# Kernel optimization log

Hardware: AMD Instinct MI355X
Metric: run time of the kernel (lower is better)

## Reference

```python
import jax, jax.numpy as jnp
import numpy as np

NEG = -9e9  # large negative used by the original torch code for masking


def setup_inputs() -> dict:
    key = jax.random.key(0)
    k1, k2, k3, k4 = jax.random.split(key, 4)
    B, N, L, D = 64, 128, 64, 768
    return {
        "text_embeddings": jax.random.normal(k1, (B, N, D), dtype=jnp.float32),
        "image_embeddings": jax.random.normal(k2, (B, L, D), dtype=jnp.float32),
        "text_mask": jax.random.randint(k3, (B, N), 0, 2, dtype=jnp.int32),
        "image_mask": jax.random.randint(k4, (B, L), 0, 2, dtype=jnp.int32),
    }


def _grounding(text_emb, image_emb, text_mask, image_mask):
    # Vectorized version of the B x B python loop in score_grounding.
    tm = text_mask.astype(text_emb.dtype)   # [B, N]
    im = image_mask.astype(text_emb.dtype)  # [B, L]
    # pairwise mask: mask[i, j, n, l] = text_mask[i, n] * image_mask[j, l]
    mask = tm[:, None, :, None] * im[None, :, None, :]            # [B, B, N, L]
    att = jnp.einsum('ind,jld->ijnl', text_emb, image_emb) * mask  # [B, B, N, L]
    att = jnp.where(att * mask != 0, att, NEG)
    # softmax over image spans (last dim), masked
    aw_first = jax.nn.softmax(att, axis=-1) * mask
    score1 = (aw_first * att).sum(-1).mean(-1)                     # [B, B]
    # softmax over text spans (dim 2 == the N axis), masked (transpose trick in torch)
    aw_second = jax.nn.softmax(att, axis=2) * mask
    score2 = (aw_second * att).sum(-1).mean(-1)                    # [B, B]
    sent_scores = score1 + score2                                  # [B, B]
    B = text_emb.shape[0]
    idx = jnp.arange(B)
    token_scores = att[idx, idx]                                   # diagonal pairs, [B, N, L]
    return sent_scores, token_scores


def reference(text_embeddings, image_embeddings, text_mask, image_mask):
    B = text_embeddings.shape[0]
    S, token_scores = _grounding(text_embeddings, image_embeddings, text_mask, image_mask)
    # text_emb_i2s = softmax(att_weights) @ image_emb
    text_emb_i2s = jnp.einsum('bnl,bld->bnd', jax.nn.softmax(token_scores, axis=-1), image_embeddings)
    # loss = -(sum diag logsoftmax(S, dim=1) + sum diag logsoftmax(S.T, dim=1)) / n
    ls1 = jnp.diagonal(jax.nn.log_softmax(S, axis=1))
    ls2 = jnp.diagonal(jax.nn.log_softmax(S.T, axis=1))
    loss = -(jnp.sum(ls1) + jnp.sum(ls2)) / B
    return loss, text_emb_i2s
```

## Files before the change

### kernel.cpp

```cpp
#include <hip/hip_runtime.h>
#include <math.h>

#define BSZ 64
#define NN  128
#define LL  64
#define DD  768
#define NEGV (-9e9f)

#define TQ (BSZ * NN * DD / 4)
#define IQ (BSZ * LL * DD / 4)

typedef _Float16 f16x8 __attribute__((ext_vector_type(8)));
typedef __attribute__((ext_vector_type(4))) float f32x4;

__device__ __forceinline__ void gl_lds16(const void* g, void* l) {
    __builtin_amdgcn_global_load_lds(
        (const __attribute__((address_space(1))) void*)g,
        (__attribute__((address_space(3))) void*)l, 16, 0, 0);
}

__global__ __launch_bounds__(256) void k_prep(
    const float4* __restrict__ t4, const float4* __restrict__ g4,
    ushort4* __restrict__ A, ushort4* __restrict__ B)
{
    int id = blockIdx.x * 256 + threadIdx.x;
    const float4* src; ushort4* dst; int idx;
    if (id < TQ) { src = t4; dst = A; idx = id; }
    else         { src = g4; dst = B; idx = id - TQ; }
    float4 x = src[idx];
    _Float16 h0 = (_Float16)x.x, h1 = (_Float16)x.y;
    _Float16 h2 = (_Float16)x.z, h3 = (_Float16)x.w;
    ushort4 o;
    o.x = __builtin_bit_cast(unsigned short, h0);
    o.y = __builtin_bit_cast(unsigned short, h1);
    o.z = __builtin_bit_cast(unsigned short, h2);
    o.w = __builtin_bit_cast(unsigned short, h3);
    dst[idx] = o;
}

__device__ __forceinline__ void stage_chunk(
    const unsigned short* __restrict__ pa, const unsigned short* __restrict__ pb,
    int k0, char* buf, int wave, int lane)
{
    int rsub = lane >> 3;
    int k8s  = lane & 7;
#pragma unroll
    for (int c = 0; c < 4; c++) {
        int r  = c * 32 + wave * 8 + rsub;
        int k8 = k8s ^ (r & 7);
        gl_lds16(pa + (size_t)r * DD + k0 + k8 * 8, buf + c * 4096 + wave * 1024);
        gl_lds16(pb + (size_t)r * DD + k0 + k8 * 8, buf + 16384 + c * 4096 + wave * 1024);
    }
}

__global__ __launch_bounds__(256, 2) void k_scores(
    const unsigned short* __restrict__ A, const unsigned short* __restrict__ B,
    const int* __restrict__ tmask, const int* __restrict__ imask,
    float* __restrict__ S, float* __restrict__ W)
{
    union SmemU {
        char  stage[2][32768];
        float Cs[NN][129];
    };
    __shared__ SmemU u;
    __shared__ float tmi[NN];
    __shared__ float imj[NN];
    __shared__ float rowred[256];
    __shared__ float colred[NN];
    __shared__ float rowm[256], rowsm[256];
    __shared__ float colm[256], colp1[256], colp2[256];

    const int bid = blockIdx.x;
    const int grp = bid >> 4, idx = bid & 15;
    const int i  = (grp >> 3) * 4 + (idx >> 2);
    const int jj = (grp & 7) * 4 + (idx & 3);
    const int j0 = jj * 2;

    const int tid  = threadIdx.x;
    const int wave = tid >> 6;
    const int lane = tid & 63;
    const int quad = lane >> 4;
    const int l15  = lane & 15;
    const int rh   = wave & 1;
    const int ch   = wave >> 1;

    if (tid < NN) {
        tmi[tid] = tmask[i * NN + tid] ? 1.f : 0.f;
        imj[tid] = imask[j0 * LL + tid] ? 1.f : 0.f;
    }

    const unsigned short* pa = A + (size_t)i * NN * DD;
    const unsigned short* pb = B + (size_t)j0 * LL * DD;

    f32x4 acc[4][4];
    const f32x4 zf = {0.f, 0.f, 0.f, 0.f};
#pragma unroll
    for (int tr = 0; tr < 4; tr++)
#pragma unroll
        for (int tc = 0; tc < 4; tc++) acc[tr][tc] = zf;

    stage_chunk(pa, pb, 0, u.stage[0], wave, lane);
    __syncthreads();

    for (int c = 0; c < 12; c++) {
        if (c + 1 < 12)
            stage_chunk(pa, pb, (c + 1) << 6, u.stage[(c + 1) & 1], wave, lane);
        const char* Ab = u.stage[c & 1];
        const char* Bb = Ab + 16384;
#pragma unroll
        for (int s = 0; s < 2; s++) {
            int k8q = s * 4 + quad;
            int sw  = k8q ^ (l15 & 7);
            f16x8 af[4], bfr[4];
#pragma unroll
            for (int t = 0; t < 4; t++) {
                int row = rh * 64 + t * 16 + l15;
                af[t]  = *(const f16x8*)(Ab + ((row << 3) + sw) * 16);
                int col = ch * 64 + t * 16 + l15;
                bfr[t] = *(const f16x8*)(Bb + ((col << 3) + sw) * 16);
            }
#pragma unroll
            for (int tr = 0; tr < 4; tr++)
#pragma unroll
                for (int tc = 0; tc < 4; tc++)
                    acc[tr][tc] = __builtin_amdgcn_mfma_f32_16x16x32_f16(
                        af[tr], bfr[tc], acc[tr][tc], 0, 0, 0);
        }
        __syncthreads();
    }

#pragma unroll
    for (int tr = 0; tr < 4; tr++) {
        int rb = rh * 64 + tr * 16 + quad * 4;
#pragma unroll
        for (int tc = 0; tc < 4; tc++) {
            int col = ch * 64 + tc * 16 + l15;
            float im = imj[col];
#pragma unroll
            for (int rr = 0; rr < 4; rr++) {
                int row = rb + rr;
                float v = acc[tr][tc][rr];
                bool keep = (tmi[row] != 0.f) && (im != 0.f) && (v != 0.f);
                u.Cs[row][col] = keep ? v : NEGV;
            }
        }
    }
    __syncthreads();

    {
        int jh = tid >> 7, n = tid & 127;
        const float* Crow = &u.Cs[n][jh * 64];
        float m = -INFINITY;
        for (int l = 0; l < LL; l++) m = fmaxf(m, Crow[l]);
        float ssum = 0.f, ws = 0.f;
        for (int l = 0; l < LL; l++) {
            float v = Crow[l];
            float e = __expf(v - m);
            ssum += e;
            ws += imj[jh * 64 + l] * e * v;
        }
        rowm[tid] = m;
        rowsm[tid] = ssum;
        rowred[tid] = tmi[n] * (ws / ssum);
    }
    __syncthreads();

    {
        int c  = tid & 127;
        int n0 = (tid >> 7) * 64;
        float m = -INFINITY;
        for (int n = n0; n < n0 + 64; n++) m = fmaxf(m, u.Cs[n][c]);
        colm[tid] = m;
        __syncthreads();
        m = fmaxf(colm[tid], colm[tid ^ 128]);
        float ssum = 0.f, ws = 0.f;
        for (int n = n0; n < n0 + 64; n++) {
            float v = u.Cs[n][c];
            float e = __expf(v - m);
            ssum += e;
            ws += tmi[n] * e * v;
        }
        colp1[tid] = ssum;
        colp2[tid] = ws;
    }
    __syncthreads();
    if (tid < NN) {
        float ssum = colp1[tid] + colp1[tid + 128];
        float ws   = colp2[tid] + colp2[tid + 128];
        colred[tid] = imj[tid] * (ws / ssum);
    }

    if (jj == (i >> 1) && tid < NN) {
        int jh = i & 1;
        int n = tid;
        float m   = rowm[jh * 128 + n];
        float inv = 1.f / rowsm[jh * 128 + n];
        const float* Crow = &u.Cs[n][jh * 64];
        float* Wb = W + (size_t)i * LL * NN;
        for (int l = 0; l < LL; l++)
            Wb[(size_t)l * NN + n] = __expf(Crow[l] - m) * inv;
    }
    __syncthreads();

    if (tid < NN) {
        int jh = tid >> 6, t = tid & 63;
        float p = rowred[jh * 128 + t] + rowred[jh * 128 + 64 + t] + colred[jh * 64 + t];
#pragma unroll
        for (int off = 32; off; off >>= 1) p += __shfl_down(p, off);
        if (t == 0) S[i * BSZ + j0 + jh] = p / (float)NN;
    }
}

__global__ __launch_bounds__(256) void k_i2s(
    const float* __restrict__ W, const float* __restrict__ img,
    float* __restrict__ out)
{
    __shared__ float Ws[LL][16];
    const int b  = blockIdx.x;
    const int ng = blockIdx.z * 16;
    const int d  = blockIdx.y * 256 + threadIdx.x;
    const float* Wb = W + (size_t)b * LL * NN;

    {
        int t4 = threadIdx.x * 4;
        int l = t4 >> 4, noff = t4 & 15;
        float4 w = *(const float4*)(Wb + (size_t)l * NN + ng + noff);
        Ws[l][noff + 0] = w.x; Ws[l][noff + 1] = w.y;
        Ws[l][noff + 2] = w.z; Ws[l][noff + 3] = w.w;
    }
    __syncthreads();

    const float* ib = img + (size_t)b * LL * DD;
    float* ob = out + 1 + (size_t)b * NN * DD + (size_t)ng * DD;

    float acc[16];
#pragma unroll
    for (int q = 0; q < 16; q++) acc[q] = 0.f;
    for (int l = 0; l < LL; l++) {
        float g = ib[(size_t)l * DD + d];
#pragma unroll
        for (int q = 0; q < 16; q++)
            acc[q] = fmaf(Ws[l][q], g, acc[q]);
    }
#pragma unroll
    for (int q = 0; q < 16; q++)
        ob[(size_t)q * DD + d] = acc[q];
}

__global__ void k_loss(const float* __restrict__ S, float* __restrict__ out)
{
    const int t = threadIdx.x;
    float diag = S[t * BSZ + t];
    float m1 = -INFINITY, m2 = -INFINITY;
    for (int jj = 0; jj < BSZ; jj++) {
        m1 = fmaxf(m1, S[t * BSZ + jj]);
        m2 = fmaxf(m2, S[jj * BSZ + t]);
    }
    float s1 = 0.f, s2 = 0.f;
    for (int jj = 0; jj < BSZ; jj++) {
        s1 += __expf(S[t * BSZ + jj] - m1);
        s2 += __expf(S[jj * BSZ + t] - m2);
    }
    float p = 2.f * diag - (m1 + logf(s1)) - (m2 + logf(s2));
#pragma unroll
    for (int off = 32; off; off >>= 1) p += __shfl_down(p, off);
    if (t == 0) out[0] = -p / (float)BSZ;
}

extern "C" void kernel_launch(void* const* d_in, const int* in_sizes, int n_in,
                              void* d_out, int out_size, void* d_ws, size_t ws_size,
                              hipStream_t stream)
{
    (void)in_sizes; (void)n_in; (void)out_size; (void)ws_size;
    const float* text = (const float*)d_in[0];
    const float* img  = (const float*)d_in[1];
    const int*   tm   = (const int*)d_in[2];
    const int*   im   = (const int*)d_in[3];
    float* out = (float*)d_out;

    char* ws = (char*)d_ws;
    unsigned short* A = (unsigned short*)(ws);
    unsigned short* B = (unsigned short*)(ws + 12582912);
    float* S = (float*)(ws + 18874368);
    float* W = (float*)(ws + 18890752);

    k_prep<<<(TQ + IQ) / 256, 256, 0, stream>>>(
        (const float4*)text, (const float4*)img, (ushort4*)A, (ushort4*)B);

    k_scores<<<BSZ * (BSZ / 2), 256, 0, stream>>>(A, B, tm, im, S, W);

    dim3 g2(BSZ, 3, 8);
    k_i2s<<<g2, 256, 0, stream>>>(W, img, out);

    k_loss<<<1, 64, 0, stream>>>(S, out);
}
```

Baseline: 188.1 us.

## Widen score tiles to four image batches per block with 512 threads

Each k_scores block now computes one text batch against four image batches (a 128x256 tile) using 8 waves instead of 4 waves over two batches. The K chunk shrinks to 32, staged in a k-major layout without the swizzle, and the block count halves. The masked softmax reductions run per image batch from a smaller 128x65 LDS buffer, split across both halves of the threads. This raises reuse of the text operand and lowers LDS use per block. The cost is more barriers in the epilogue, a serialized loop over four image batches, and possible LDS bank conflicts from the unswizzled layout.

```diff
diff --git a/kernel.cpp b/kernel.cpp
--- a/kernel.cpp
+++ b/kernel.cpp
@@ -42,52 +42,53 @@
     const unsigned short* __restrict__ pa, const unsigned short* __restrict__ pb,
     int k0, char* buf, int wave, int lane)
 {
-    int rsub = lane >> 3;
-    int k8s  = lane & 7;
-#pragma unroll
-    for (int c = 0; c < 4; c++) {
-        int r  = c * 32 + wave * 8 + rsub;
-        int k8 = k8s ^ (r & 7);
-        gl_lds16(pa + (size_t)r * DD + k0 + k8 * 8, buf + c * 4096 + wave * 1024);
-        gl_lds16(pb + (size_t)r * DD + k0 + k8 * 8, buf + 16384 + c * 4096 + wave * 1024);
-    }
-}
-
-__global__ __launch_bounds__(256, 2) void k_scores(
+    int s = wave * 64 + lane;
+    {
+        int k8 = s >> 7, r = s & 127;
+        gl_lds16(pa + (size_t)r * DD + k0 + k8 * 8, buf + wave * 1024);
+    }
+    {
+        int k8 = s >> 8, c = s & 255;
+        gl_lds16(pb + (size_t)c * DD + k0 + k8 * 8, buf + 8192 + wave * 1024);
+    }
+    {
+        int s2 = s + 512;
+        int k8 = s2 >> 8, c = s2 & 255;
+        gl_lds16(pb + (size_t)c * DD + k0 + k8 * 8, buf + 16384 + wave * 1024);
+    }
+}
+
+__global__ __launch_bounds__(512, 6) void k_scores(
     const unsigned short* __restrict__ A, const unsigned short* __restrict__ B,
     const int* __restrict__ tmask, const int* __restrict__ imask,
     float* __restrict__ S, float* __restrict__ W)
 {
     union SmemU {
-        char  stage[2][32768];
-        float Cs[NN][129];
+        char  stage[2][24576];
+        float Cs[NN][65];
     };
     __shared__ SmemU u;
     __shared__ float tmi[NN];
-    __shared__ float imj[NN];
-    __shared__ float rowred[256];
-    __shared__ float colred[NN];
-    __shared__ float rowm[256], rowsm[256];
-    __shared__ float colm[256], colp1[256], colp2[256];
+    __shared__ float imj[256];
+    __shared__ float rowm[NN], rowsm[NN], rowred[NN];
+    __shared__ float colred[LL];
 
     const int bid = blockIdx.x;
     const int grp = bid >> 4, idx = bid & 15;
-    const int i  = (grp >> 3) * 4 + (idx >> 2);
-    const int jj = (grp & 7) * 4 + (idx & 3);
-    const int j0 = jj * 2;
+    const int i   = (grp >> 2) * 4 + (idx >> 2);
+    const int jj4 = (grp & 3) * 4 + (idx & 3);
+    const int j0  = jj4 * 4;
 
     const int tid  = threadIdx.x;
     const int wave = tid >> 6;
     const int lane = tid & 63;
     const int quad = lane >> 4;
     const int l15  = lane & 15;
-    const int rh   = wave & 1;
-    const int ch   = wave >> 1;
-
-    if (tid < NN) {
-        tmi[tid] = tmask[i * NN + tid] ? 1.f : 0.f;
-        imj[tid] = imask[j0 * LL + tid] ? 1.f : 0.f;
-    }
+    const int wr   = wave & 1;
+    const int wc   = wave >> 1;
+
+    if (tid < NN)       tmi[tid] = tmask[i * NN + tid] ? 1.f : 0.f;
+    else if (tid < 384) imj[tid - NN] = imask[j0 * LL + (tid - NN)] ? 1.f : 0.f;
 
     const unsigned short* pa = A + (size_t)i * NN * DD;
     const unsigned short* pb = B + (size_t)j0 * LL * DD;
@@ -102,112 +103,115 @@
     stage_chunk(pa, pb, 0, u.stage[0], wave, lane);
     __syncthreads();
 
-    for (int c = 0; c < 12; c++) {
-        if (c + 1 < 12)
-            stage_chunk(pa, pb, (c + 1) << 6, u.stage[(c + 1) & 1], wave, lane);
+    for (int c = 0; c < 24; c++) {
+        if (c + 1 < 24)
+            stage_chunk(pa, pb, (c + 1) << 5, u.stage[(c + 1) & 1], wave, lane);
         const char* Ab = u.stage[c & 1];
-        const char* Bb = Ab + 16384;
-#pragma unroll
-        for (int s = 0; s < 2; s++) {
-            int k8q = s * 4 + quad;
-            int sw  = k8q ^ (l15 & 7);
-            f16x8 af[4], bfr[4];
-#pragma unroll
-            for (int t = 0; t < 4; t++) {
-                int row = rh * 64 + t * 16 + l15;
-                af[t]  = *(const f16x8*)(Ab + ((row << 3) + sw) * 16);
-                int col = ch * 64 + t * 16 + l15;
-                bfr[t] = *(const f16x8*)(Bb + ((col << 3) + sw) * 16);
+        const char* Bb = Ab + 8192;
+        f16x8 af[4], bfr[4];
+#pragma unroll
+        for (int t = 0; t < 4; t++) {
+            af[t]  = *(const f16x8*)(Ab + ((quad << 7) + wr * 64 + t * 16 + l15) * 16);
+            bfr[t] = *(const f16x8*)(Bb + ((quad << 8) + wc * 64 + t * 16 + l15) * 16);
+        }
+#pragma unroll
+        for (int tr = 0; tr < 4; tr++)
+#pragma unroll
+            for (int tc = 0; tc < 4; tc++)
+                acc[tr][tc] = __builtin_amdgcn_mfma_f32_16x16x32_f16(
+                    af[tr], bfr[tc], acc[tr][tc], 0, 0, 0);
+        __syncthreads();
+    }
+
+    float imv[4];
+#pragma unroll
+    for (int tc = 0; tc < 4; tc++) imv[tc] = imj[wc * 64 + tc * 16 + l15];
+#pragma unroll
+    for (int tr = 0; tr < 4; tr++) {
+#pragma unroll
+        for (int rr = 0; rr < 4; rr++) {
+            float tmv = tmi[wr * 64 + tr * 16 + quad * 4 + rr];
+#pragma unroll
+            for (int tc = 0; tc < 4; tc++) {
+                float v = acc[tr][tc][rr];
+                bool keep = (tmv != 0.f) && (imv[tc] != 0.f) && (v != 0.f);
+                acc[tr][tc][rr] = keep ? v : NEGV;
             }
+        }
+    }
+
+    const bool diag = (jj4 == (i >> 2));
+    const int  jhd  = i & 3;
+    float* Cs = &u.Cs[0][0];
+
+    for (int jh = 0; jh < 4; jh++) {
+        __syncthreads();
+        if (wc == jh) {
 #pragma unroll
             for (int tr = 0; tr < 4; tr++)
 #pragma unroll
                 for (int tc = 0; tc < 4; tc++)
-                    acc[tr][tc] = __builtin_amdgcn_mfma_f32_16x16x32_f16(
-                        af[tr], bfr[tc], acc[tr][tc], 0, 0, 0);
+#pragma unroll
+                    for (int rr = 0; rr < 4; rr++)
+                        Cs[(wr * 64 + tr * 16 + quad * 4 + rr) * 65 + tc * 16 + l15]
+                            = acc[tr][tc][rr];
         }
         __syncthreads();
-    }
-
-#pragma unroll
-    for (int tr = 0; tr < 4; tr++) {
-        int rb = rh * 64 + tr * 16 + quad * 4;
-#pragma unroll
-        for (int tc = 0; tc < 4; tc++) {
-            int col = ch * 64 + tc * 16 + l15;
-            float im = imj[col];
-#pragma unroll
-            for (int rr = 0; rr < 4; rr++) {
-                int row = rb + rr;
-                float v = acc[tr][tc][rr];
-                bool keep = (tmi[row] != 0.f) && (im != 0.f) && (v != 0.f);
-                u.Cs[row][col] = keep ? v : NEGV;
+
+        if (tid < 256) {
+            int row = tid >> 1, off = (tid & 1) * 32;
+            const float* Cr = Cs + row * 65 + off;
+            float m = -INFINITY;
+            for (int l = 0; l < 32; l++) m = fmaxf(m, Cr[l]);
+            m = fmaxf(m, __shfl_xor(m, 1));
+            float ssum = 0.f, ws = 0.f;
+            for (int l = 0; l < 32; l++) {
+                float v = Cr[l];
+                float e = __expf(v - m);
+                ssum += e;
+                ws += imj[jh * 64 + off + l] * e * v;
             }
-        }
-    }
-    __syncthreads();
-
-    {
-        int jh = tid >> 7, n = tid & 127;
-        const float* Crow = &u.Cs[n][jh * 64];
-        float m = -INFINITY;
-        for (int l = 0; l < LL; l++) m = fmaxf(m, Crow[l]);
-        float ssum = 0.f, ws = 0.f;
-        for (int l = 0; l < LL; l++) {
-            float v = Crow[l];
-            float e = __expf(v - m);
-            ssum += e;
-            ws += imj[jh * 64 + l] * e * v;
-        }
-        rowm[tid] = m;
-        rowsm[tid] = ssum;
-        rowred[tid] = tmi[n] * (ws / ssum);
-    }
-    __syncthreads();
-
-    {
-        int c  = tid & 127;
-        int n0 = (tid >> 7) * 64;
-        float m = -INFINITY;
-        for (int n = n0; n < n0 + 64; n++) m = fmaxf(m, u.Cs[n][c]);
-        colm[tid] = m;
+            ssum += __shfl_xor(ssum, 1);
+            ws   += __shfl_xor(ws, 1);
+            if ((tid & 1) == 0) {
+                rowm[row]  = m;
+                rowsm[row] = ssum;
+                rowred[row] = tmi[row] * (ws / ssum);
+            }
+        } else {
+            int u2 = tid - 256;
+            int col = u2 >> 2, n0 = (u2 & 3) * 32;
+            float m = -INFINITY;
+            for (int n = 0; n < 32; n++) m = fmaxf(m, Cs[(n0 + n) * 65 + col]);
+            m = fmaxf(m, __shfl_xor(m, 1));
+            m = fmaxf(m, __shfl_xor(m, 2));
+            float ssum = 0.f, ws = 0.f;
+            for (int n = 0; n < 32; n++) {
+                float v = Cs[(n0 + n) * 65 + col];
+                float e = __expf(v - m);
+                ssum += e;
+                ws += tmi[n0 + n] * e * v;
+            }
+            ssum += __shfl_xor(ssum, 1); ssum += __shfl_xor(ssum, 2);
+            ws   += __shfl_xor(ws, 1);   ws   += __shfl_xor(ws, 2);
+            if ((u2 & 3) == 0) colred[col] = imj[jh * 64 + col] * (ws / ssum);
+        }
         __syncthreads();
-        m = fmaxf(colm[tid], colm[tid ^ 128]);
-        float ssum = 0.f, ws = 0.f;
-        for (int n = n0; n < n0 + 64; n++) {
-            float v = u.Cs[n][c];
-            float e = __expf(v - m);
-            ssum += e;
-            ws += tmi[n] * e * v;
-        }
-        colp1[tid] = ssum;
-        colp2[tid] = ws;
-    }
-    __syncthreads();
-    if (tid < NN) {
-        float ssum = colp1[tid] + colp1[tid + 128];
-        float ws   = colp2[tid] + colp2[tid + 128];
-        colred[tid] = imj[tid] * (ws / ssum);
-    }
-
-    if (jj == (i >> 1) && tid < NN) {
-        int jh = i & 1;
-        int n = tid;
-        float m   = rowm[jh * 128 + n];
-        float inv = 1.f / rowsm[jh * 128 + n];
-        const float* Crow = &u.Cs[n][jh * 64];
-        float* Wb = W + (size_t)i * LL * NN;
-        for (int l = 0; l < LL; l++)
-            Wb[(size_t)l * NN + n] = __expf(Crow[l] - m) * inv;
-    }
-    __syncthreads();
-
-    if (tid < NN) {
-        int jh = tid >> 6, t = tid & 63;
-        float p = rowred[jh * 128 + t] + rowred[jh * 128 + 64 + t] + colred[jh * 64 + t];
-#pragma unroll
-        for (int off = 32; off; off >>= 1) p += __shfl_down(p, off);
-        if (t == 0) S[i * BSZ + j0 + jh] = p / (float)NN;
+
+        if (tid < 64) {
+            float p = rowred[tid] + rowred[64 + tid] + colred[tid];
+#pragma unroll
+            for (int off = 32; off; off >>= 1) p += __shfl_down(p, off);
+            if (tid == 0) S[i * BSZ + j0 + jh] = p / (float)NN;
+        } else if (diag && jh == jhd && tid >= 128 && tid < 384) {
+            int dn = tid - 128;
+            int n = dn >> 1, l0 = (dn & 1) * 32;
+            float m   = rowm[n];
+            float inv = 1.f / rowsm[n];
+            float* Wb = W + (size_t)i * LL * NN;
+            for (int l = 0; l < 32; l++)
+                Wb[(size_t)(l0 + l) * NN + n] = __expf(Cs[n * 65 + l0 + l] - m) * inv;
+        }
     }
 }
 
@@ -287,7 +291,7 @@
     k_prep<<<(TQ + IQ) / 256, 256, 0, stream>>>(
         (const float4*)text, (const float4*)img, (ushort4*)A, (ushort4*)B);
 
-    k_scores<<<BSZ * (BSZ / 2), 256, 0, stream>>>(A, B, tm, im, S, W);
+    k_scores<<<BSZ * (BSZ / 4), 512, 0, stream>>>(A, B, tm, im, S, W);
 
     dim3 g2(BSZ, 3, 8);
     k_i2s<<<g2, 256, 0, stream>>>(W, img, out);
```

Result: slower. 593.1 us (+215.3%).
